# Performance work log

Measured on AMD Instinct MI355X. Metric: run time of the kernel, lower is better.

The kernel has to match this reference:

```python
import jax, jax.numpy as jnp
import numpy as np

N = 50000      # nodes (full graph: num_dst == num_src == N)
E = 800000     # edges, avg degree 16
D = 128        # in_feats == n_hidden == out_feats
L = 3          # n_layers
EPS = 1e-5     # BatchNorm1d eps


def setup_inputs() -> dict:
    key = jax.random.key(0)
    ks = jax.random.split(key, 6)
    feat = jax.random.normal(ks[0], (N, D), dtype=jnp.float32)
    src = jax.random.randint(ks[1], (E,), 0, N)
    dst = jax.random.randint(ks[2], (E,), 0, N)
    scale = 1.0 / np.sqrt(D)
    W_self = jax.random.normal(ks[3], (L, D, D), dtype=jnp.float32) * scale
    W_neigh = jax.random.normal(ks[4], (L, D, D), dtype=jnp.float32) * scale
    b = jax.random.normal(ks[5], (L, D), dtype=jnp.float32) * 0.01
    gamma = jnp.ones((L - 1, D), dtype=jnp.float32)
    beta = jnp.zeros((L - 1, D), dtype=jnp.float32)
    return {"feat": feat, "src": src, "dst": dst, "W_self": W_self,
            "W_neigh": W_neigh, "b": b, "gamma": gamma, "beta": beta}


def reference(feat, src, dst, W_self, W_neigh, b, gamma, beta):
    n = feat.shape[0]
    n_layers = W_self.shape[0]
    # in-degree of each dst node, clamped to 1 (zero-degree nodes aggregate 0)
    deg = jax.ops.segment_sum(jnp.ones_like(dst, dtype=feat.dtype), dst,
                              num_segments=n)
    deg = jnp.maximum(deg, 1.0)[:, None]                      # [N,1]
    h = feat
    for i in range(n_layers):
        # mean aggregation over incoming neighbors: gather + segment-sum
        agg = jax.ops.segment_sum(h[src], dst, num_segments=n) / deg  # [N,D]
        # SAGEConv('mean'): fc_self(h_dst) + fc_neigh(agg) + bias
        hn = h @ W_self[i] + agg @ W_neigh[i] + b[i]
        hn = hn + h                                           # residual (dims match)
        if i < n_layers - 1:
            mu = jnp.mean(hn, axis=0)
            var = jnp.var(hn, axis=0)                         # biased, as BN training
            hn = (hn - mu) * jax.lax.rsqrt(var + EPS) * gamma[i] + beta[i]
            hn = jax.nn.relu(hn)
        h = hn
    return h
```

## Files before the change

kernel.cpp:

```cpp
#include <hip/hip_runtime.h>

#define DIM 128
#define EPSF 1e-5f
#define BK_SHIFT 8
#define BK_NODES 256
#define GRP_SHIFT 13
#define NGRP 8
#define BKS_CAP 1536
#define MAXNBS 1600

typedef __attribute__((ext_vector_type(8))) short short8;
typedef __attribute__((ext_vector_type(4))) float float4v;

__device__ inline unsigned short f2bf(float x) {
    union { float f; unsigned u; } z; z.f = x;
    unsigned u = z.u;
    unsigned r = u + 0x7FFF + ((u >> 16) & 1);
    return (unsigned short)(r >> 16);
}
__device__ inline float bf2f(unsigned short u) {
    union { unsigned u; float f; } z; z.u = ((unsigned)u) << 16;
    return z.f;
}

__global__ void binA_kernel(const int* __restrict__ src, const int* __restrict__ dst,
                            unsigned* __restrict__ barr, int* __restrict__ bcnt,
                            int E, int NBS) {
    __shared__ int cnt[MAXNBS];
    __shared__ int gcur[MAXNBS];
    int tid = threadIdx.x;
    int tile0 = blockIdx.x * 4096;
    for (int j = tid; j < NBS; j += 256) cnt[j] = 0;
    __syncthreads();
    unsigned pk[16]; int bk[16];
#pragma unroll
    for (int i = 0; i < 16; ++i) {
        int e = tile0 + i * 256 + tid;
        if (e < E) {
            int d = dst[e];
            int s = src[e];
            bk[i] = ((d >> BK_SHIFT) << 3) | (s >> GRP_SHIFT);
            pk[i] = ((unsigned)(d & (BK_NODES - 1)) << 16) | (unsigned)s;
            atomicAdd(&cnt[bk[i]], 1);
        } else bk[i] = -1;
    }
    __syncthreads();
    for (int j = tid; j < NBS; j += 256) {
        int c = cnt[j];
        gcur[j] = (c > 0) ? atomicAdd(&bcnt[j], c) : 0;
    }
    __syncthreads();
#pragma unroll
    for (int i = 0; i < 16; ++i) {
        if (bk[i] >= 0) {
            int pos = atomicAdd(&gcur[bk[i]], 1);
            if (pos < BKS_CAP)
                barr[(size_t)bk[i] * BKS_CAP + pos] = pk[i];
        }
    }
}

__global__ void binB_kernel(const unsigned* __restrict__ barr, const int* __restrict__ bcnt,
                            int* __restrict__ rowptr, int* __restrict__ colidx,
                            int N, int E, int NBS) {
    __shared__ int hist[256];
    __shared__ int sm[256];
    __shared__ int bc[NGRP];
    int b = blockIdx.x;
    int tid = threadIdx.x;
    int lim = b * NGRP;
    int part = 0;
    for (int i = tid; i < lim; i += 256) part += bcnt[i];
    sm[tid] = part;
    if (tid < NGRP) bc[tid] = bcnt[lim + tid];
    __syncthreads();
    for (int off = 128; off > 0; off >>= 1) {
        if (tid < off) sm[tid] += sm[tid + off];
        __syncthreads();
    }
    int gb = sm[0];
    if (b == 0 && tid == 0) rowptr[N] = E;
    __syncthreads();
    hist[tid] = 0;
    __syncthreads();
    for (int g = 0; g < NGRP; ++g) {
        int cg = bc[g]; if (cg > BKS_CAP) cg = BKS_CAP;
        const unsigned* arr = barr + (size_t)(b * NGRP + g) * BKS_CAP;
        for (int i = tid; i < cg; i += 256)
            atomicAdd(&hist[arr[i] >> 16], 1);
    }
    __syncthreads();
    int h = hist[tid];
    sm[tid] = h;
    __syncthreads();
    for (int off = 1; off < 256; off <<= 1) {
        int x = (tid >= off) ? sm[tid - off] : 0;
        __syncthreads();
        sm[tid] += x;
        __syncthreads();
    }
    int base = sm[tid] - h;
    hist[tid] = base;
    int node = (b << BK_SHIFT) + tid;
    if (node < N) rowptr[node] = gb + base;
    __syncthreads();
    for (int g = 0; g < NGRP; ++g) {
        int cg = bc[g]; if (cg > BKS_CAP) cg = BKS_CAP;
        const unsigned* arr = barr + (size_t)(b * NGRP + g) * BKS_CAP;
        for (int i = tid; i < cg; i += 256) {
            unsigned u = arr[i];
            int pos = atomicAdd(&hist[u >> 16], 1);
            colidx[gb + pos] = (int)(u & 0xFFFFu);
        }
        __syncthreads();
    }
}

__global__ void prep_kernel(const float* __restrict__ Ws, const float* __restrict__ Wn,
                            unsigned short* __restrict__ wpack,
                            const float* __restrict__ feat, unsigned short* __restrict__ Hb,
                            int* __restrict__ zbase, int N) {
    int b = blockIdx.x;
    int tid = threadIdx.x;
    if (b < 24) {
        int l = b >> 3;
        int s = b & 7;
#pragma unroll
        for (int pi = 0; pi < 2; ++pi) {
            int p = tid * 2 + pi;
            int nt = p >> 6;
            int lane = p & 63;
            int kb = s * 32 + (lane >> 4) * 8;
            int col = nt * 16 + (lane & 15);
            unsigned short* dstp = wpack + (size_t)l * 32768 + ((size_t)(s * 8 + nt) * 64 + lane) * 8;
#pragma unroll
            for (int j = 0; j < 8; ++j) {
                int k = kb + j;
                float v = (k < 128) ? Ws[(size_t)l * 16384 + k * 128 + col]
                                    : Wn[(size_t)l * 16384 + (k - 128) * 128 + col];
                dstp[j] = f2bf(v);
            }
        }
        return;
    }
    if (b == 24) {
        for (int j = tid; j < MAXNBS + 512; j += 256) zbase[j] = 0;
        return;
    }
    int idx = (b - 25) * 256 + tid;
    if (idx >= N * 32) return;
    float4 v = ((const float4*)feat)[idx];
    ushort4 o;
    o.x = f2bf(v.x); o.y = f2bf(v.y); o.z = f2bf(v.z); o.w = f2bf(v.w);
    ((ushort4*)Hb)[idx] = o;
}

__global__ void aggregate_kernel(const unsigned short* __restrict__ Hb,
                                 unsigned short* __restrict__ Agg,
                                 const int* __restrict__ rowptr,
                                 const int* __restrict__ colidx, int N) {
    int wid = (blockIdx.x * blockDim.x + threadIdx.x) >> 6;
    if (wid >= N) return;
    int lane = threadIdx.x & 63;
    int half = lane >> 5, sl = lane & 31;
    int beg = rowptr[wid], end = rowptr[wid + 1];
    float4 acc = make_float4(0.f, 0.f, 0.f, 0.f);
    int e = beg + half;
    for (; e + 6 < end; e += 8) {
        int s0 = colidx[e];
        int s1 = colidx[e + 2];
        int s2 = colidx[e + 4];
        int s3 = colidx[e + 6];
        ushort4 u0 = *(const ushort4*)(Hb + (size_t)s0 * 128 + sl * 4);
        ushort4 u1 = *(const ushort4*)(Hb + (size_t)s1 * 128 + sl * 4);
        ushort4 u2 = *(const ushort4*)(Hb + (size_t)s2 * 128 + sl * 4);
        ushort4 u3 = *(const ushort4*)(Hb + (size_t)s3 * 128 + sl * 4);
        acc.x += (bf2f(u0.x) + bf2f(u1.x)) + (bf2f(u2.x) + bf2f(u3.x));
        acc.y += (bf2f(u0.y) + bf2f(u1.y)) + (bf2f(u2.y) + bf2f(u3.y));
        acc.z += (bf2f(u0.z) + bf2f(u1.z)) + (bf2f(u2.z) + bf2f(u3.z));
        acc.w += (bf2f(u0.w) + bf2f(u1.w)) + (bf2f(u2.w) + bf2f(u3.w));
    }
    for (; e < end; e += 2) {
        int s0 = colidx[e];
        ushort4 u0 = *(const ushort4*)(Hb + (size_t)s0 * 128 + sl * 4);
        acc.x += bf2f(u0.x);
        acc.y += bf2f(u0.y);
        acc.z += bf2f(u0.z);
        acc.w += bf2f(u0.w);
    }
    acc.x += __shfl_xor(acc.x, 32);
    acc.y += __shfl_xor(acc.y, 32);
    acc.z += __shfl_xor(acc.z, 32);
    acc.w += __shfl_xor(acc.w, 32);
    if (half == 0) {
        int deg = end - beg;
        float inv = 1.0f / (float)(deg > 0 ? deg : 1);
        ushort4 o;
        o.x = f2bf(acc.x * inv); o.y = f2bf(acc.y * inv);
        o.z = f2bf(acc.z * inv); o.w = f2bf(acc.w * inv);
        *(ushort4*)(Agg + (size_t)wid * 128 + sl * 4) = o;
    }
}

__launch_bounds__(256)
__global__ void gemm_kernel(const unsigned short* __restrict__ Hb,
                            const unsigned short* __restrict__ Agg,
                            const unsigned short* __restrict__ wpack,
                            const float* __restrict__ bias,
                            unsigned short* __restrict__ outb, float* __restrict__ outf,
                            float* __restrict__ stats, int withStats, int N) {
    __shared__ unsigned short Bs[32768];
    int tid = threadIdx.x;
    {
        const float4* wsrc = (const float4*)wpack;
        float4* bdst = (float4*)Bs;
#pragma unroll
        for (int i = 0; i < 16; ++i) bdst[i * 256 + tid] = wsrc[i * 256 + tid];
    }
    __syncthreads();

    int wave = tid >> 6, lane = tid & 63;
    int row0 = blockIdx.x * 128 + wave * 32;
    int mrow = lane & 15, kq = lane >> 4;
    const unsigned short* Sbase = Hb + (size_t)(row0 + mrow) * 128 + kq * 8;
    const unsigned short* Gbase = Agg + (size_t)(row0 + mrow) * 128 + kq * 8;

    float4v acc[2][8];
#pragma unroll
    for (int i = 0; i < 2; ++i)
#pragma unroll
        for (int j = 0; j < 8; ++j) acc[i][j] = (float4v){0.f, 0.f, 0.f, 0.f};

#pragma unroll
    for (int s = 0; s < 8; ++s) {
        const unsigned short* ab = (s < 4) ? (Sbase + s * 32) : (Gbase + (s - 4) * 32);
        short8 a0 = *(const short8*)ab;
        short8 a1 = *(const short8*)(ab + 16 * 128);
#pragma unroll
        for (int nt = 0; nt < 8; ++nt) {
            short8 b = *(const short8*)(Bs + ((size_t)(s * 8 + nt) * 64 + lane) * 8);
            acc[0][nt] = __builtin_amdgcn_mfma_f32_16x16x32_bf16(a0, b, acc[0][nt], 0, 0, 0);
            acc[1][nt] = __builtin_amdgcn_mfma_f32_16x16x32_bf16(a1, b, acc[1][nt], 0, 0, 0);
        }
    }

    float* sm = (float*)Bs;
    if (withStats) {
        __syncthreads();
        sm[tid] = 0.f;
        __syncthreads();
    }

    int colb = lane & 15;
    int rq = (lane >> 4) * 4;
#pragma unroll
    for (int mt = 0; mt < 2; ++mt) {
        int rowt = row0 + mt * 16 + rq;
#pragma unroll
        for (int nt = 0; nt < 8; ++nt) {
            int col = nt * 16 + colb;
            float bv = bias[col];
            float slo = 0.f, qlo = 0.f;
#pragma unroll
            for (int r = 0; r < 4; ++r) {
                int row = rowt + r;
                if (row < N) {
                    float res = bf2f(Hb[(size_t)row * 128 + col]);
                    float v = acc[mt][nt][r] + bv + res;
                    if (withStats) {
                        outb[(size_t)row * 128 + col] = f2bf(v);
                        slo += v; qlo += v * v;
                    } else {
                        outf[(size_t)row * 128 + col] = v;
                    }
                }
            }
            if (withStats) {
                atomicAdd(&sm[col], slo);
                atomicAdd(&sm[128 + col], qlo);
            }
        }
    }
    if (withStats) {
        __syncthreads();
        if (tid < 128) {
            atomicAdd(&stats[tid], sm[tid]);
            atomicAdd(&stats[128 + tid], sm[128 + tid]);
        }
    }
}

__global__ void bn_kernel(const unsigned short* __restrict__ hn,
                          unsigned short* __restrict__ Hb,
                          const float* __restrict__ stats, const float* __restrict__ gamma,
                          const float* __restrict__ beta, float invN, int N) {
    __shared__ float sc_s[128], sh_s[128];
    int tid = threadIdx.x;
    if (tid < 128) {
        float mean = stats[tid] * invN;
        float var = stats[128 + tid] * invN - mean * mean;
        float sc = gamma[tid] * rsqrtf(var + EPSF);
        sc_s[tid] = sc;
        sh_s[tid] = beta[tid] - mean * sc;
    }
    __syncthreads();
    int idx = blockIdx.x * 256 + tid;
    if (idx >= N * 32) return;
    int c4 = idx & 31;
    ushort4 u = *(const ushort4*)(hn + (size_t)idx * 4);
    ushort4 o;
    {
        int col = c4 * 4;
        float v0 = fmaf(bf2f(u.x), sc_s[col], sh_s[col]);
        float v1 = fmaf(bf2f(u.y), sc_s[col + 1], sh_s[col + 1]);
        float v2 = fmaf(bf2f(u.z), sc_s[col + 2], sh_s[col + 2]);
        float v3 = fmaf(bf2f(u.w), sc_s[col + 3], sh_s[col + 3]);
        o.x = f2bf(fmaxf(v0, 0.f));
        o.y = f2bf(fmaxf(v1, 0.f));
        o.z = f2bf(fmaxf(v2, 0.f));
        o.w = f2bf(fmaxf(v3, 0.f));
    }
    *(ushort4*)(Hb + (size_t)idx * 4) = o;
}

extern "C" void kernel_launch(void* const* d_in, const int* in_sizes, int n_in,
                              void* d_out, int out_size, void* d_ws, size_t ws_size,
                              hipStream_t stream) {
    const float* feat  = (const float*)d_in[0];
    const int*   src   = (const int*)d_in[1];
    const int*   dst   = (const int*)d_in[2];
    const float* Wself = (const float*)d_in[3];
    const float* Wneig = (const float*)d_in[4];
    const float* bias  = (const float*)d_in[5];
    const float* gamma = (const float*)d_in[6];
    const float* beta  = (const float*)d_in[7];

    int N = in_sizes[0] / DIM;
    int E = in_sizes[1];
    int Npad = (N + 127) & ~127;
    int NB = (N + BK_NODES - 1) >> BK_SHIFT;
    int NBS = NB * NGRP;

    char* ws = (char*)d_ws;
    size_t off = 0;
    auto alloc = [&](size_t bytes) -> void* {
        void* p = ws + off;
        off = (off + bytes + 255) & ~(size_t)255;
        return p;
    };
    unsigned short* Hb    = (unsigned short*)alloc((size_t)Npad * 128 * 2);
    unsigned short* Agg   = (unsigned short*)alloc((size_t)Npad * 128 * 2);
    unsigned short* Hd    = (unsigned short*)alloc((size_t)Npad * 128 * 2);
    unsigned short* wpack = (unsigned short*)alloc((size_t)3 * 32768 * 2);
    int*   colidx = (int*)alloc((size_t)E * 4);
    int*   rowptr = (int*)alloc((size_t)(N + 1) * 4);
    int*   bcnt   = (int*)alloc(MAXNBS * 4);
    float* stats  = (float*)alloc(512 * 4);

    unsigned* barr = (unsigned*)Agg;

    float invN = 1.0f / (float)N;
    int nagg = (N + 3) / 4;
    int nbn  = (N * 32 + 255) / 256;

    prep_kernel<<<25 + nbn, 256, 0, stream>>>(Wself, Wneig, wpack, feat, Hb, bcnt, N);
    binA_kernel<<<(E + 4095) / 4096, 256, 0, stream>>>(src, dst, barr, bcnt, E, NBS);
    binB_kernel<<<NB, 256, 0, stream>>>(barr, bcnt, rowptr, colidx, N, E, NBS);

    aggregate_kernel<<<nagg, 256, 0, stream>>>(Hb, Agg, rowptr, colidx, N);
    gemm_kernel<<<Npad / 128, 256, 0, stream>>>(Hb, Agg, wpack, bias,
                                                Hd, (float*)d_out, stats, 1, N);
    bn_kernel<<<nbn, 256, 0, stream>>>(Hd, Hb, stats, gamma, beta, invN, N);
    aggregate_kernel<<<nagg, 256, 0, stream>>>(Hb, Agg, rowptr, colidx, N);
    gemm_kernel<<<Npad / 128, 256, 0, stream>>>(Hb, Agg, wpack + 32768, bias + DIM,
                                                Hd, (float*)d_out, stats + 256, 1, N);
    bn_kernel<<<nbn, 256, 0, stream>>>(Hd, Hb, stats + 256, gamma + DIM, beta + DIM, invN, N);
    aggregate_kernel<<<nagg, 256, 0, stream>>>(Hb, Agg, rowptr, colidx, N);
    gemm_kernel<<<Npad / 128, 256, 0, stream>>>(Hb, Agg, wpack + 2 * 32768, bias + 2 * DIM,
                                                Hd, (float*)d_out, stats, 0, N);
}
```

Baseline: 333.3 us.

## Use 16-bit column indices, wider aggregate gathers, and drop LDS weight staging

Column indices are stored as 16-bit values, since node ids were already packed into 16 bits; this halves index traffic. The aggregate kernel now splits each wave into four 16-lane groups, each loading 16 bytes per lane, so four edges are gathered at once with wider loads and then combined with two shuffles. The GEMM kernel stops copying the 64KB packed weights into LDS and reads B fragments straight from global memory (L2/L1). This removes the LDS fill and barrier and raises occupancy, at the cost of more repeated cache reads of the weights. The 16-bit indices only work while node count stays at or below 65536.

Result: slower. 346.5 us (+4.0%).

```diff
diff --git a/kernel.cpp b/kernel.cpp
--- a/kernel.cpp
+++ b/kernel.cpp
@@ -10,6 +10,7 @@
 #define MAXNBS 1600
 
 typedef __attribute__((ext_vector_type(8))) short short8;
+typedef __attribute__((ext_vector_type(8))) unsigned short ushort8;
 typedef __attribute__((ext_vector_type(4))) float float4v;
 
 __device__ inline unsigned short f2bf(float x) {
@@ -61,7 +62,7 @@
 }
 
 __global__ void binB_kernel(const unsigned* __restrict__ barr, const int* __restrict__ bcnt,
-                            int* __restrict__ rowptr, int* __restrict__ colidx,
+                            int* __restrict__ rowptr, unsigned short* __restrict__ colidx,
                             int N, int E, int NBS) {
     __shared__ int hist[256];
     __shared__ int sm[256];
@@ -110,7 +111,7 @@
         for (int i = tid; i < cg; i += 256) {
             unsigned u = arr[i];
             int pos = atomicAdd(&hist[u >> 16], 1);
-            colidx[gb + pos] = (int)(u & 0xFFFFu);
+            colidx[gb + pos] = (unsigned short)(u & 0xFFFFu);
         }
         __syncthreads();
     }
@@ -158,47 +159,48 @@
 __global__ void aggregate_kernel(const unsigned short* __restrict__ Hb,
                                  unsigned short* __restrict__ Agg,
                                  const int* __restrict__ rowptr,
-                                 const int* __restrict__ colidx, int N) {
+                                 const unsigned short* __restrict__ colidx, int N) {
     int wid = (blockIdx.x * blockDim.x + threadIdx.x) >> 6;
     if (wid >= N) return;
     int lane = threadIdx.x & 63;
-    int half = lane >> 5, sl = lane & 31;
+    int q = lane >> 4, ql = lane & 15;
     int beg = rowptr[wid], end = rowptr[wid + 1];
-    float4 acc = make_float4(0.f, 0.f, 0.f, 0.f);
-    int e = beg + half;
-    for (; e + 6 < end; e += 8) {
+    float a[8];
+#pragma unroll
+    for (int j = 0; j < 8; ++j) a[j] = 0.f;
+    int e = beg + q;
+    for (; e + 12 < end; e += 16) {
         int s0 = colidx[e];
-        int s1 = colidx[e + 2];
-        int s2 = colidx[e + 4];
-        int s3 = colidx[e + 6];
-        ushort4 u0 = *(const ushort4*)(Hb + (size_t)s0 * 128 + sl * 4);
-        ushort4 u1 = *(const ushort4*)(Hb + (size_t)s1 * 128 + sl * 4);
-        ushort4 u2 = *(const ushort4*)(Hb + (size_t)s2 * 128 + sl * 4);
-        ushort4 u3 = *(const ushort4*)(Hb + (size_t)s3 * 128 + sl * 4);
-        acc.x += (bf2f(u0.x) + bf2f(u1.x)) + (bf2f(u2.x) + bf2f(u3.x));
-        acc.y += (bf2f(u0.y) + bf2f(u1.y)) + (bf2f(u2.y) + bf2f(u3.y));
-        acc.z += (bf2f(u0.z) + bf2f(u1.z)) + (bf2f(u2.z) + bf2f(u3.z));
-        acc.w += (bf2f(u0.w) + bf2f(u1.w)) + (bf2f(u2.w) + bf2f(u3.w));
-    }
-    for (; e < end; e += 2) {
+        int s1 = colidx[e + 4];
+        int s2 = colidx[e + 8];
+        int s3 = colidx[e + 12];
+        ushort8 u0 = *(const ushort8*)(Hb + (size_t)s0 * 128 + ql * 8);
+        ushort8 u1 = *(const ushort8*)(Hb + (size_t)s1 * 128 + ql * 8);
+        ushort8 u2 = *(const ushort8*)(Hb + (size_t)s2 * 128 + ql * 8);
+        ushort8 u3 = *(const ushort8*)(Hb + (size_t)s3 * 128 + ql * 8);
+#pragma unroll
+        for (int j = 0; j < 8; ++j)
+            a[j] += (bf2f((unsigned short)u0[j]) + bf2f((unsigned short)u1[j]))
+                  + (bf2f((unsigned short)u2[j]) + bf2f((unsigned short)u3[j]));
+    }
+    for (; e < end; e += 4) {
         int s0 = colidx[e];
-        ushort4 u0 = *(const ushort4*)(Hb + (size_t)s0 * 128 + sl * 4);
-        acc.x += bf2f(u0.x);
-        acc.y += bf2f(u0.y);
-        acc.z += bf2f(u0.z);
-        acc.w += bf2f(u0.w);
-    }
-    acc.x += __shfl_xor(acc.x, 32);
-    acc.y += __shfl_xor(acc.y, 32);
-    acc.z += __shfl_xor(acc.z, 32);
-    acc.w += __shfl_xor(acc.w, 32);
-    if (half == 0) {
+        ushort8 u0 = *(const ushort8*)(Hb + (size_t)s0 * 128 + ql * 8);
+#pragma unroll
+        for (int j = 0; j < 8; ++j) a[j] += bf2f((unsigned short)u0[j]);
+    }
+#pragma unroll
+    for (int j = 0; j < 8; ++j) {
+        a[j] += __shfl_xor(a[j], 16);
+        a[j] += __shfl_xor(a[j], 32);
+    }
+    if (q == 0) {
         int deg = end - beg;
         float inv = 1.0f / (float)(deg > 0 ? deg : 1);
-        ushort4 o;
-        o.x = f2bf(acc.x * inv); o.y = f2bf(acc.y * inv);
-        o.z = f2bf(acc.z * inv); o.w = f2bf(acc.w * inv);
-        *(ushort4*)(Agg + (size_t)wid * 128 + sl * 4) = o;
+        ushort8 o;
+#pragma unroll
+        for (int j = 0; j < 8; ++j) o[j] = f2bf(a[j] * inv);
+        *(ushort8*)(Agg + (size_t)wid * 128 + ql * 8) = o;
     }
 }
 
@@ -209,15 +211,9 @@
                             const float* __restrict__ bias,
                             unsigned short* __restrict__ outb, float* __restrict__ outf,
                             float* __restrict__ stats, int withStats, int N) {
-    __shared__ unsigned short Bs[32768];
-    int tid = threadIdx.x;
-    {
-        const float4* wsrc = (const float4*)wpack;
-        float4* bdst = (float4*)Bs;
-#pragma unroll
-        for (int i = 0; i < 16; ++i) bdst[i * 256 + tid] = wsrc[i * 256 + tid];
-    }
-    __syncthreads();
+    __shared__ float sm[256];
+    int tid = threadIdx.x;
+    if (withStats) sm[tid] = 0.f;
 
     int wave = tid >> 6, lane = tid & 63;
     int row0 = blockIdx.x * 128 + wave * 32;
@@ -238,18 +234,13 @@
         short8 a1 = *(const short8*)(ab + 16 * 128);
 #pragma unroll
         for (int nt = 0; nt < 8; ++nt) {
-            short8 b = *(const short8*)(Bs + ((size_t)(s * 8 + nt) * 64 + lane) * 8);
+            short8 b = *(const short8*)(wpack + ((size_t)(s * 8 + nt) * 64 + lane) * 8);
             acc[0][nt] = __builtin_amdgcn_mfma_f32_16x16x32_bf16(a0, b, acc[0][nt], 0, 0, 0);
             acc[1][nt] = __builtin_amdgcn_mfma_f32_16x16x32_bf16(a1, b, acc[1][nt], 0, 0, 0);
         }
     }
 
-    float* sm = (float*)Bs;
-    if (withStats) {
-        __syncthreads();
-        sm[tid] = 0.f;
-        __syncthreads();
-    }
+    if (withStats) __syncthreads();
 
     int colb = lane & 15;
     int rq = (lane >> 4) * 4;
@@ -352,7 +343,7 @@
     unsigned short* Agg   = (unsigned short*)alloc((size_t)Npad * 128 * 2);
     unsigned short* Hd    = (unsigned short*)alloc((size_t)Npad * 128 * 2);
     unsigned short* wpack = (unsigned short*)alloc((size_t)3 * 32768 * 2);
-    int*   colidx = (int*)alloc((size_t)E * 4);
+    unsigned short* colidx = (unsigned short*)alloc((size_t)E * 2);
     int*   rowptr = (int*)alloc((size_t)(N + 1) * 4);
     int*   bcnt   = (int*)alloc(MAXNBS * 4);
     float* stats  = (float*)alloc(512 * 4);
```
